# Kernel optimization log

Measured on AMD Instinct MI355X. Metric: run time of the kernel, lower is better.

The kernel has to match this reference:

```python
import math
import jax, jax.numpy as jnp
import numpy as np

N_TOKENS = 2048
HIDDEN = 2880
HEAD_DIM = 64
N_HEADS = 64          # total attention heads
N_KV = 8              # key/value heads
Q_MULT = N_HEADS // N_KV
SLIDING_WINDOW = 128  # layer_idx=0 (even) -> window active
ROPE_BASE = 150000.0
INIT_CTX = 4096.0
ROPE_SCALE = 32.0
NTK_ALPHA = 1.0
NTK_BETA = 32.0
QKV_DIM = HEAD_DIM * (N_HEADS + 2 * N_KV)  # 5120
EPS = 1e-5
NEG = -1e30


def _cos_sin(n_tokens):
    # YaRN-scaled rotary tables (scaling_factor > 1 branch)
    freq = ROPE_BASE ** (jnp.arange(0, HEAD_DIM, 2, dtype=jnp.float32) / HEAD_DIM)
    concentration = 0.1 * jnp.log(jnp.float32(ROPE_SCALE)) + 1.0
    d_half = HEAD_DIM / 2
    log_base = jnp.log(jnp.float32(ROPE_BASE))
    low = d_half * jnp.log(jnp.float32(INIT_CTX / (NTK_BETA * 2 * np.pi))) / log_base
    high = d_half * jnp.log(jnp.float32(INIT_CTX / (NTK_ALPHA * 2 * np.pi))) / log_base
    interpolation = 1.0 / (ROPE_SCALE * freq)
    extrapolation = 1.0 / freq
    ramp = (jnp.arange(d_half, dtype=jnp.float32) - low) / (high - low)
    mask = 1.0 - jnp.clip(ramp, 0.0, 1.0)
    inv_freq = interpolation * (1.0 - mask) + extrapolation * mask
    t = jnp.arange(n_tokens, dtype=jnp.float32)
    freqs = t[:, None] * inv_freq[None, :]          # [n, head_dim//2]
    return jnp.cos(freqs) * concentration, jnp.sin(freqs) * concentration


def _apply_rotary(x, cos, sin):
    # x: [n, heads, head_dim]; cos/sin: [n, head_dim//2]
    cos = cos[:, None, :].astype(x.dtype)
    sin = sin[:, None, :].astype(x.dtype)
    x1, x2 = jnp.split(x, 2, axis=-1)
    return jnp.concatenate((x1 * cos - x2 * sin, x2 * cos + x1 * sin), axis=-1)


def _rmsnorm(x, scale):
    t = x.astype(jnp.float32)
    rms = jnp.sqrt(jnp.mean(t * t, axis=-1, keepdims=True) + EPS)
    return (t / rms * scale).astype(x.dtype)


def _sdpa(q, k, v, sinks):
    # q: [n, h_kv, q_mult, d]; k, v: [n, h_kv, d]; sinks: [n_heads]
    n = q.shape[0]
    sm_scale = 1.0 / math.sqrt(HEAD_DIM)
    q32, k32, v32 = q.astype(jnp.float32), k.astype(jnp.float32), v.astype(jnp.float32)
    qk = jnp.einsum('qhmd,khd->hmqk', q32, k32) * jnp.float32(sm_scale)
    i = jnp.arange(n)
    # causal AND within sliding window: q - window < k <= q
    allowed = (i[None, :] <= i[:, None]) & (i[None, :] > i[:, None] - SLIDING_WINDOW)
    qk = qk + jnp.where(allowed, jnp.float32(0.0), jnp.float32(NEG))[None, None, :, :]
    s = sinks.astype(jnp.float32).reshape(N_KV, Q_MULT, 1, 1)
    s = jnp.broadcast_to(s, (N_KV, Q_MULT, n, 1))
    w = jax.nn.softmax(jnp.concatenate([qk, s], axis=-1), axis=-1)[..., :-1]
    attn = jnp.einsum('hmqk,khd->qhmd', w, v32)
    return attn.astype(q.dtype).reshape(n, -1)  # [n, n_heads*head_dim]


def setup_inputs() -> dict:
    key = jax.random.key(0)
    ks = jax.random.split(key, 5)
    s = 0.02
    return {
        'x': jax.random.normal(ks[0], (N_TOKENS, HIDDEN), jnp.float32),
        'norm_scale': jnp.ones((HIDDEN,), jnp.float32),
        'w_qkv': jax.random.normal(ks[1], (HIDDEN, QKV_DIM), jnp.float32) * s,
        'b_qkv': jnp.zeros((QKV_DIM,), jnp.float32),
        'sinks': jax.random.normal(ks[2], (N_HEADS,), jnp.float32),
        'w_out': jax.random.normal(ks[3], (N_HEADS * HEAD_DIM, HIDDEN), jnp.float32) * s,
        'b_out': jnp.zeros((HIDDEN,), jnp.float32),
    }


def reference(x, norm_scale, w_qkv, b_qkv, sinks, w_out, b_out):
    n = x.shape[0]
    t = _rmsnorm(x, norm_scale)
    qkv = t @ w_qkv + b_qkv                                   # [n, qkv_dim]
    q_end = N_HEADS * HEAD_DIM
    k_end = q_end + N_KV * HEAD_DIM
    q = qkv[:, :q_end].reshape(n, N_KV, Q_MULT, HEAD_DIM)
    k = qkv[:, q_end:k_end].reshape(n, N_KV, HEAD_DIM)
    v = qkv[:, k_end:].reshape(n, N_KV, HEAD_DIM)
    cos, sin = _cos_sin(n)
    q = _apply_rotary(q.reshape(n, -1, HEAD_DIM), cos, sin).reshape(n, N_KV, Q_MULT, HEAD_DIM)
    k = _apply_rotary(k, cos, sin)
    attn = _sdpa(q, k, v, sinks)                              # [n, n_heads*head_dim]
    return x + (attn @ w_out + b_out)
```

## Files before the change

kernel.cpp:

```cpp
#include <hip/hip_runtime.h>
#include <hip/hip_bf16.h>
#include <math.h>

#define N_TOK 2048
#define HIDDEN 2880
#define QKV_DIM 5120
#define LOG2E 1.44269504088896340736f

typedef __attribute__((ext_vector_type(8))) short short8;
typedef __attribute__((ext_vector_type(4))) float f32x4;
typedef __attribute__((ext_vector_type(16))) float f32x16;

__device__ __forceinline__ float bf2f(unsigned short u) {
  union { unsigned int i; float f; } c; c.i = ((unsigned int)u) << 16; return c.f;
}
__device__ __forceinline__ unsigned short f2bf(float f) {
  union { float f; unsigned int i; } c; c.f = f;
  unsigned int i = c.i;
  return (unsigned short)((i + 0x7FFFu + ((i >> 16) & 1u)) >> 16);
}
__device__ __forceinline__ void gload16(const void* g, void* l) {
  __builtin_amdgcn_global_load_lds((const __attribute__((address_space(1))) void*)g,
                                   (__attribute__((address_space(3))) void*)l, 16, 0, 0);
}

__global__ __launch_bounds__(256) void rmsnorm_kernel(
    const float* __restrict__ x, const float* __restrict__ scale,
    unsigned short* __restrict__ t)
{
  int row = blockIdx.x;
  const float* xr = x + (size_t)row * HIDDEN;
  float ss = 0.f;
  for (int i = threadIdx.x; i < HIDDEN / 4; i += 256) {
    float4 v = ((const float4*)xr)[i];
    ss += v.x * v.x + v.y * v.y + v.z * v.z + v.w * v.w;
  }
#pragma unroll
  for (int off = 32; off; off >>= 1) ss += __shfl_down(ss, off, 64);
  __shared__ float red[4];
  if ((threadIdx.x & 63) == 0) red[threadIdx.x >> 6] = ss;
  __syncthreads();
  float total = red[0] + red[1] + red[2] + red[3];
  float rinv = rsqrtf(total / (float)HIDDEN + 1e-5f);
  for (int i = threadIdx.x; i < HIDDEN / 4; i += 256) {
    float4 v = ((const float4*)xr)[i];
    float4 s4 = ((const float4*)scale)[i];
    union { unsigned short u[4]; uint2 p; } pk;
    pk.u[0] = f2bf(v.x * rinv * s4.x);
    pk.u[1] = f2bf(v.y * rinv * s4.y);
    pk.u[2] = f2bf(v.z * rinv * s4.z);
    pk.u[3] = f2bf(v.w * rinv * s4.w);
    *(uint2*)&t[(size_t)row * HIDDEN + i * 4] = pk.p;
  }
}

__global__ __launch_bounds__(256) void transpose_cast2(
    const float* __restrict__ inA, unsigned short* __restrict__ outA,
    const float* __restrict__ inB, unsigned short* __restrict__ outB)
{
  __shared__ float tile[64][65];
  int b = blockIdx.x;
  const float* in; unsigned short* out; int R, C, bx, by;
  if (b < 3600) { in = inA; out = outA; R = 2880; C = 5120; bx = b % 80; by = b / 80; }
  else { b -= 3600; in = inB; out = outB; R = 4096; C = 2880; bx = b % 45; by = b / 45; }
  const int r0 = by * 64, c0 = bx * 64;
  const int t = threadIdx.x;
  const int c4 = t & 15, rr = t >> 4;
#pragma unroll
  for (int p = 0; p < 4; ++p) {
    int row = rr + p * 16;
    float4 v = *(const float4*)&in[(size_t)(r0 + row) * C + c0 + c4 * 4];
    tile[row][c4 * 4 + 0] = v.x; tile[row][c4 * 4 + 1] = v.y;
    tile[row][c4 * 4 + 2] = v.z; tile[row][c4 * 4 + 3] = v.w;
  }
  __syncthreads();
  const int rc = t & 7;
#pragma unroll
  for (int it = 0; it < 2; ++it) {
    int cc = (t >> 3) + it * 32;
    unsigned short tmp[8];
#pragma unroll
    for (int i = 0; i < 8; ++i) tmp[i] = f2bf(tile[rc * 8 + i][cc]);
    *(uint4*)&out[(size_t)(c0 + cc) * R + r0 + rc * 8] = *(uint4*)tmp;
  }
}

template <int NF, int EPI>
__global__ __launch_bounds__(512, 2) void gemm8(
    const unsigned short* __restrict__ A,
    const unsigned short* __restrict__ Bt,
    const float* __restrict__ bias,
    const float* __restrict__ resid,
    void* __restrict__ Cout,
    int K, int Ncols)
{
  constexpr int BUFSZ = 16384 + NF * 8192;
  constexpr int NCH = 2 + NF;
  constexpr int HALF = NCH / 2;
  __shared__ char smem_[2 * BUFSZ];
  const int tid = threadIdx.x;
  const int lane = tid & 63;
  const int w = tid >> 6;
  const int fr = lane & 15, fq = lane >> 4;
  const int wr = w >> 2, wc = w & 3;

  const int nwg = gridDim.x;
  const int cpx = nwg >> 3;
  const int wg = (blockIdx.x & 7) * cpx + (blockIdx.x >> 3);
  const int by = wg & 15, bx = wg >> 4;
  const int row0 = by * 128, col0 = bx * (NF * 64);

  const unsigned short* gsrc[NCH];
  int ldsoff[NCH];
#pragma unroll
  for (int c = 0; c < NCH; ++c) {
    int g = tid + 512 * c;
    if (g < 1024) {
      int kk = g >> 9, rr = (g >> 2) & 127, u = g & 3;
      gsrc[c] = A + (size_t)(row0 + rr) * K + kk * 32 + ((u ^ ((rr >> 1) & 3)) * 8);
      ldsoff[c] = kk * 8192 + rr * 64 + u * 16;
    } else {
      int g2 = g - 1024;
      int kk = g2 / (NF * 256);
      int rm = g2 - kk * (NF * 256);
      int rr = rm >> 2, u = rm & 3;
      gsrc[c] = Bt + (size_t)(col0 + rr) * K + kk * 32 + ((u ^ ((rr >> 1) & 3)) * 8);
      ldsoff[c] = 16384 + kk * (NF * 4096) + rr * 64 + u * 16;
    }
  }
  const int urd = (fq ^ ((fr >> 1) & 3)) * 16;
  const int aoffb = (wr * 64 + fr) * 64 + urd;
  const int boffb = 16384 + (wc * NF * 16 + fr) * 64 + urd;

  f32x4 acc[4][NF];
#pragma unroll
  for (int mf = 0; mf < 4; ++mf)
#pragma unroll
    for (int nf = 0; nf < NF; ++nf) acc[mf][nf] = (f32x4)0.f;

  const int NT = K >> 6;

#define ISSUE(c) gload16(gsrc[c] + ktn, smem_ + nbufo + ldsoff[c])
#define RD_A(mf, kk) (*(const short8*)(smem_ + bufo + (kk)*8192 + (mf)*1024 + aoffb))
#define RD_B(nf, kk) (*(const short8*)(smem_ + bufo + (kk)*(NF*4096) + (nf)*1024 + boffb))

  {
    const int ktn = 0, nbufo = 0;
#pragma unroll
    for (int c = 0; c < NCH; ++c) gload16(gsrc[c] + ktn, smem_ + nbufo + ldsoff[c]);
  }

  for (int t = 0; t < NT; ++t) {
    const int bufo = (t & 1) * BUFSZ;
    const int nbufo = bufo ^ BUFSZ;
    const int ktn = (t + 1) * 64;
    const bool pref = (t + 1) < NT;

    asm volatile("s_waitcnt vmcnt(0)" ::: "memory");
    __builtin_amdgcn_s_barrier();

    if (pref) {
#pragma unroll
      for (int c = 0; c < HALF; ++c) ISSUE(c);
    }

    short8 afr[4], bfr[NF];
#pragma unroll
    for (int nf = 0; nf < NF; ++nf) bfr[nf] = RD_B(nf, 0);
#pragma unroll
    for (int mf = 0; mf < 4; ++mf) afr[mf] = RD_A(mf, 0);
    __builtin_amdgcn_s_setprio(1);
#pragma unroll
    for (int mf = 0; mf < 4; ++mf)
#pragma unroll
      for (int nf = 0; nf < NF; ++nf)
        acc[mf][nf] = __builtin_amdgcn_mfma_f32_16x16x32_bf16(afr[mf], bfr[nf], acc[mf][nf], 0, 0, 0);
    __builtin_amdgcn_s_setprio(0);

    if (pref) {
#pragma unroll
      for (int c = HALF; c < NCH; ++c) ISSUE(c);
    }

#pragma unroll
    for (int nf = 0; nf < NF; ++nf) bfr[nf] = RD_B(nf, 1);
#pragma unroll
    for (int mf = 0; mf < 4; ++mf) afr[mf] = RD_A(mf, 1);
    __builtin_amdgcn_s_setprio(1);
#pragma unroll
    for (int mf = 0; mf < 4; ++mf)
#pragma unroll
      for (int nf = 0; nf < NF; ++nf)
        acc[mf][nf] = __builtin_amdgcn_mfma_f32_16x16x32_bf16(afr[mf], bfr[nf], acc[mf][nf], 0, 0, 0);
    __builtin_amdgcn_s_setprio(0);
  }
#undef ISSUE
#undef RD_A
#undef RD_B

#pragma unroll
  for (int mf = 0; mf < 4; ++mf) {
#pragma unroll
    for (int nf = 0; nf < NF; ++nf) {
      const int colb = col0 + wc * NF * 16 + nf * 16 + fr;
      const int rowb = row0 + wr * 64 + mf * 16 + fq * 4;
      const float bs = bias[colb];
      if (EPI == 1) {
#pragma unroll
        for (int j = 0; j < 4; ++j)
          ((unsigned short*)Cout)[(size_t)(rowb + j) * Ncols + colb] =
              f2bf(acc[mf][nf][j] + bs);
      } else {
#pragma unroll
        for (int j = 0; j < 4; ++j) {
          const size_t idx = (size_t)(rowb + j) * Ncols + colb;
          ((float*)Cout)[idx] = acc[mf][nf][j] + bs + resid[idx];
        }
      }
    }
  }
}

__global__ __launch_bounds__(256) void rope_kernel(unsigned short* __restrict__ qkv)
{
  __shared__ float cs[32], sn[32];
  const int token = blockIdx.x;
  const int t = threadIdx.x;
  if (t < 32) {
    const float log_base = 11.9183905731f;
    float fj = (float)t;
    float extrap = expf(-log_base * fj * 0.03125f);
    float interp = extrap * 0.03125f;
    const float low  = 32.f * logf(4096.f / (32.f * 6.283185307179586f)) / log_base;
    const float high = 32.f * logf(4096.f / 6.283185307179586f) / log_base;
    float ramp = (fj - low) / (high - low);
    float maskv = 1.f - fminf(fmaxf(ramp, 0.f), 1.f);
    float inv_freq = interp * (1.f - maskv) + extrap * maskv;
    float ang = (float)token * inv_freq;
    const float conc = 1.3465735903f;
    float s, c;
    sincosf(ang, &s, &c);
    cs[t] = c * conc; sn[t] = s * conc;
  }
  __syncthreads();
  for (int p = t; p < 72 * 32; p += 256) {
    int h = p >> 5, j = p & 31;
    size_t base = (size_t)token * QKV_DIM + h * 64 + j;
    float c = cs[j], s = sn[j];
    float x1 = bf2f(qkv[base]), x2 = bf2f(qkv[base + 32]);
    qkv[base]      = f2bf(x1 * c - x2 * s);
    qkv[base + 32] = f2bf(x2 * c + x1 * s);
  }
}

__global__ __launch_bounds__(512) void attn_kernel(
    const unsigned short* __restrict__ qkv, const float* __restrict__ sinks,
    unsigned short* __restrict__ attn)
{
  __shared__ unsigned short Ks[160 * 64];
  __shared__ unsigned short Vt[64 * 192];
  const int tid  = threadIdx.x;
  const int lane = tid & 63;
  const int w    = tid >> 6;
  const int qb = blockIdx.x, kvh = blockIdx.y;
  const int q0 = qb * 32;
  const int kb = q0 - 128;
  const int h  = lane >> 5;
  const int ql = lane & 31;

  for (int it = w; it < 20; it += 8) {
    int r = it * 8 + (lane >> 3);
    int s = lane & 7;
    int j = kb + r; if (j < 0) j = 0;
    const unsigned short* src =
        qkv + (size_t)j * QKV_DIM + 4096 + kvh * 64 + ((s ^ (r & 7)) * 8);
    gload16(src, &Ks[r * 64 + s * 8]);
  }
  for (int c = tid; c < 2560; c += 512) {
    int jl = c >> 4;
    int d4 = (c & 15) * 4;
    int j = kb + jl; if (j < 0) j = 0;
    ushort4 v4 = *(const ushort4*)&qkv[(size_t)j * QKV_DIM + 4608 + kvh * 64 + d4];
    const unsigned short* pv = (const unsigned short*)&v4;
#pragma unroll
    for (int t = 0; t < 4; ++t) {
      int d = d4 + t;
      int slot = (jl >> 3) ^ (d & 7);
      Vt[d * 192 + slot * 8 + (jl & 7)] = pv[t];
    }
  }
  const int head = kvh * 8 + w;
  const int i_q = q0 + ql;
  short8 qf[4];
  {
    const unsigned short* qp = qkv + (size_t)i_q * QKV_DIM + head * 64 + h * 8;
#pragma unroll
    for (int ks = 0; ks < 4; ++ks) qf[ks] = *(const short8*)(qp + ks * 16);
  }
  __syncthreads();

  const float SC = 0.125f * LOG2E;
  f32x16 oacc0 = (f32x16)(0.f), oacc1 = (f32x16)(0.f);
  float m = -1e30f, l = 0.f;

  const int tstart = qb < 4 ? 4 - qb : 0;
  for (int tt = tstart; tt < 5; ++tt) {
    const int j0 = kb + tt * 32;
    f32x16 sacc = (f32x16)(0.f);
    const int kr = tt * 32 + ql;
#pragma unroll
    for (int ks = 0; ks < 4; ++ks) {
      short8 kf = *(const short8*)&Ks[kr * 64 + (((ks * 2 + h) ^ (kr & 7)) * 8)];
      sacc = __builtin_amdgcn_mfma_f32_32x32x16_bf16(kf, qf[ks], sacc, 0, 0, 0);
    }
    float sc16[16];
    float mt = -INFINITY;
#pragma unroll
    for (int e = 0; e < 16; ++e) {
      int kk = (e & 3) + 8 * (e >> 2) + 4 * h;
      int j = j0 + kk;
      float s2 = sacc[e] * SC;
      bool valid = (j <= i_q) && (j > i_q - 128);
      s2 = valid ? s2 : -INFINITY;
      sc16[e] = s2;
      mt = fmaxf(mt, s2);
    }
    mt = fmaxf(mt, __shfl_xor(mt, 32));
    float mnew = fmaxf(m, mt);
    float r = exp2f(m - mnew);
    l *= r;
    oacc0 *= r;
    oacc1 *= r;
    m = mnew;
    unsigned int wpk[8];
    float ls = 0.f;
#pragma unroll
    for (int e2 = 0; e2 < 8; ++e2) {
      float plo = exp2f(sc16[2 * e2]     - m);
      float phi = exp2f(sc16[2 * e2 + 1] - m);
      ls += plo + phi;
      asm("v_cvt_pk_bf16_f32 %0, %1, %2" : "=v"(wpk[e2]) : "v"(plo), "v"(phi));
    }
    l += ls;
#pragma unroll
    for (int m16 = 0; m16 < 2; ++m16) {
      int go = 2 * m16 + h;
      int gs = 2 * m16 + 1 - h;
      unsigned int x0 = (unsigned int)__shfl_xor((int)wpk[2 * gs],     32);
      unsigned int x1 = (unsigned int)__shfl_xor((int)wpk[2 * gs + 1], 32);
      union { unsigned int u[4]; short8 s; } bu;
      bu.u[0] = h ? x0 : wpk[2 * go];
      bu.u[1] = h ? x1 : wpk[2 * go + 1];
      bu.u[2] = h ? wpk[2 * go]     : x0;
      bu.u[3] = h ? wpk[2 * go + 1] : x1;
      short8 bfrag = bu.s;
#pragma unroll
      for (int dt = 0; dt < 2; ++dt) {
        int d = dt * 32 + ql;
        int slot = (tt * 4 + m16 * 2 + h) ^ (d & 7);
        short8 vf = *(const short8*)&Vt[d * 192 + slot * 8];
        if (dt == 0)
          oacc0 = __builtin_amdgcn_mfma_f32_32x32x16_bf16(vf, bfrag, oacc0, 0, 0, 0);
        else
          oacc1 = __builtin_amdgcn_mfma_f32_32x32x16_bf16(vf, bfrag, oacc1, 0, 0, 0);
      }
    }
  }
  float lt = l + __shfl_xor(l, 32);
  lt += exp2f(sinks[head] * LOG2E - m);
  float inv = 1.f / lt;
  unsigned short* op = attn + (size_t)i_q * 4096 + head * 64;
#pragma unroll
  for (int dt = 0; dt < 2; ++dt) {
#pragma unroll
    for (int g = 0; g < 4; ++g) {
      float f0, f1, f2, f3;
      if (dt == 0) {
        f0 = oacc0[4 * g]; f1 = oacc0[4 * g + 1]; f2 = oacc0[4 * g + 2]; f3 = oacc0[4 * g + 3];
      } else {
        f0 = oacc1[4 * g]; f1 = oacc1[4 * g + 1]; f2 = oacc1[4 * g + 2]; f3 = oacc1[4 * g + 3];
      }
      unsigned int u0, u1;
      asm("v_cvt_pk_bf16_f32 %0, %1, %2" : "=v"(u0) : "v"(f0 * inv), "v"(f1 * inv));
      asm("v_cvt_pk_bf16_f32 %0, %1, %2" : "=v"(u1) : "v"(f2 * inv), "v"(f3 * inv));
      int d = dt * 32 + 8 * g + 4 * h;
      uint2 pr; pr.x = u0; pr.y = u1;
      *(uint2*)(op + d) = pr;
    }
  }
}

extern "C" void kernel_launch(void* const* d_in, const int* in_sizes, int n_in,
                              void* d_out, int out_size, void* d_ws, size_t ws_size,
                              hipStream_t stream)
{
  const float* x      = (const float*)d_in[0];
  const float* nscale = (const float*)d_in[1];
  const float* w_qkv  = (const float*)d_in[2];
  const float* b_qkv  = (const float*)d_in[3];
  const float* sinks  = (const float*)d_in[4];
  const float* w_out  = (const float*)d_in[5];
  const float* b_out  = (const float*)d_in[6];

  char* ws = (char*)d_ws;
  unsigned short* t_bf  = (unsigned short*)(ws);
  unsigned short* wqkvT = (unsigned short*)(ws + 11796480);
  unsigned short* qkv   = (unsigned short*)(ws + 41287680);
  unsigned short* attn  = (unsigned short*)(ws + 62259200);
  unsigned short* woutT = (unsigned short*)(ws + 79036416);

  rmsnorm_kernel<<<N_TOK, 256, 0, stream>>>(x, nscale, t_bf);
  transpose_cast2<<<6480, 256, 0, stream>>>(w_qkv, wqkvT, w_out, woutT);
  gemm8<5, 1><<<256, 512, 0, stream>>>(t_bf, wqkvT, b_qkv, nullptr, (void*)qkv, 2880, 5120);
  rope_kernel<<<N_TOK, 256, 0, stream>>>(qkv);
  attn_kernel<<<dim3(64, 8), 512, 0, stream>>>(qkv, sinks, attn);
  gemm8<3, 2><<<240, 512, 0, stream>>>(attn, woutT, b_out, x, d_out, 4096, 2880);
}
```

Measured before the change: 187.0 us.

## Load GEMM B operand directly from global into registers, bypassing LDS

The GEMM no longer stages the weight (B) tile through shared memory. Each wave loads its B fragments straight from global memory into registers, double-buffered across iterations through a manually unrolled lambda body, and only A still goes through LDS. This cuts the shared-memory footprint and LDS read traffic for B. The cost is that each wave fetches B with uncoalesced-ish per-lane 16-byte loads, and B rows shared by waves in the same column are re-read from global/L2 instead of being reused from LDS.

Measured after the change: 326.1 us. 1.74x slower.

```diff
diff --git a/kernel.cpp b/kernel.cpp
--- a/kernel.cpp
+++ b/kernel.cpp
@@ -86,7 +86,7 @@
 }
 
 template <int NF, int EPI>
-__global__ __launch_bounds__(512, 2) void gemm8(
+__global__ __launch_bounds__(512, 2) void gemm9(
     const unsigned short* __restrict__ A,
     const unsigned short* __restrict__ Bt,
     const float* __restrict__ bias,
@@ -94,10 +94,7 @@
     void* __restrict__ Cout,
     int K, int Ncols)
 {
-  constexpr int BUFSZ = 16384 + NF * 8192;
-  constexpr int NCH = 2 + NF;
-  constexpr int HALF = NCH / 2;
-  __shared__ char smem_[2 * BUFSZ];
+  __shared__ char smem_[32768];
   const int tid = threadIdx.x;
   const int lane = tid & 63;
   const int w = tid >> 6;
@@ -110,27 +107,22 @@
   const int by = wg & 15, bx = wg >> 4;
   const int row0 = by * 128, col0 = bx * (NF * 64);
 
-  const unsigned short* gsrc[NCH];
-  int ldsoff[NCH];
-#pragma unroll
-  for (int c = 0; c < NCH; ++c) {
+  const unsigned short* gsrcA[2];
+  int ldsoffA[2];
+#pragma unroll
+  for (int c = 0; c < 2; ++c) {
     int g = tid + 512 * c;
-    if (g < 1024) {
-      int kk = g >> 9, rr = (g >> 2) & 127, u = g & 3;
-      gsrc[c] = A + (size_t)(row0 + rr) * K + kk * 32 + ((u ^ ((rr >> 1) & 3)) * 8);
-      ldsoff[c] = kk * 8192 + rr * 64 + u * 16;
-    } else {
-      int g2 = g - 1024;
-      int kk = g2 / (NF * 256);
-      int rm = g2 - kk * (NF * 256);
-      int rr = rm >> 2, u = rm & 3;
-      gsrc[c] = Bt + (size_t)(col0 + rr) * K + kk * 32 + ((u ^ ((rr >> 1) & 3)) * 8);
-      ldsoff[c] = 16384 + kk * (NF * 4096) + rr * 64 + u * 16;
-    }
+    int kk = g >> 9, rr = (g >> 2) & 127, u = g & 3;
+    gsrcA[c] = A + (size_t)(row0 + rr) * K + kk * 32 + ((u ^ ((rr >> 1) & 3)) * 8);
+    ldsoffA[c] = kk * 8192 + rr * 64 + u * 16;
   }
   const int urd = (fq ^ ((fr >> 1) & 3)) * 16;
   const int aoffb = (wr * 64 + fr) * 64 + urd;
-  const int boffb = 16384 + (wc * NF * 16 + fr) * 64 + urd;
+
+  const unsigned short* Brow[NF];
+#pragma unroll
+  for (int nf = 0; nf < NF; ++nf)
+    Brow[nf] = Bt + (size_t)(col0 + wc * NF * 16 + nf * 16 + fr) * K + fq * 8;
 
   f32x4 acc[4][NF];
 #pragma unroll
@@ -140,63 +132,57 @@
 
   const int NT = K >> 6;
 
-#define ISSUE(c) gload16(gsrc[c] + ktn, smem_ + nbufo + ldsoff[c])
-#define RD_A(mf, kk) (*(const short8*)(smem_ + bufo + (kk)*8192 + (mf)*1024 + aoffb))
-#define RD_B(nf, kk) (*(const short8*)(smem_ + bufo + (kk)*(NF*4096) + (nf)*1024 + boffb))
-
-  {
-    const int ktn = 0, nbufo = 0;
-#pragma unroll
-    for (int c = 0; c < NCH; ++c) gload16(gsrc[c] + ktn, smem_ + nbufo + ldsoff[c]);
-  }
-
-  for (int t = 0; t < NT; ++t) {
-    const int bufo = (t & 1) * BUFSZ;
-    const int nbufo = bufo ^ BUFSZ;
-    const int ktn = (t + 1) * 64;
-    const bool pref = (t + 1) < NT;
-
+  short8 bA[NF * 2], bB[NF * 2];
+
+#pragma unroll
+  for (int c = 0; c < 2; ++c) gload16(gsrcA[c], smem_ + ldsoffA[c]);
+#pragma unroll
+  for (int nf = 0; nf < NF; ++nf) {
+    bA[nf * 2 + 0] = *(const short8*)(Brow[nf] + 0);
+    bA[nf * 2 + 1] = *(const short8*)(Brow[nf] + 32);
+  }
+
+  auto body = [&](int T, short8 (&BC)[NF * 2], short8 (&BN)[NF * 2]) {
+    const int bufo = (T & 1) * 16384;
+    const int nbufo = bufo ^ 16384;
+    const int ktn = (T + 1) * 64;
     asm volatile("s_waitcnt vmcnt(0)" ::: "memory");
     __builtin_amdgcn_s_barrier();
-
-    if (pref) {
-#pragma unroll
-      for (int c = 0; c < HALF; ++c) ISSUE(c);
-    }
-
-    short8 afr[4], bfr[NF];
-#pragma unroll
-    for (int nf = 0; nf < NF; ++nf) bfr[nf] = RD_B(nf, 0);
-#pragma unroll
-    for (int mf = 0; mf < 4; ++mf) afr[mf] = RD_A(mf, 0);
+    if (T + 1 < NT) {
+#pragma unroll
+      for (int c = 0; c < 2; ++c) gload16(gsrcA[c] + ktn, smem_ + nbufo + ldsoffA[c]);
+#pragma unroll
+      for (int nf = 0; nf < NF; ++nf) {
+        BN[nf * 2 + 0] = *(const short8*)(Brow[nf] + ktn);
+        BN[nf * 2 + 1] = *(const short8*)(Brow[nf] + ktn + 32);
+      }
+    }
+    short8 afr[4];
+#pragma unroll
+    for (int mf = 0; mf < 4; ++mf)
+      afr[mf] = *(const short8*)(smem_ + bufo + mf * 1024 + aoffb);
     __builtin_amdgcn_s_setprio(1);
 #pragma unroll
     for (int mf = 0; mf < 4; ++mf)
 #pragma unroll
       for (int nf = 0; nf < NF; ++nf)
-        acc[mf][nf] = __builtin_amdgcn_mfma_f32_16x16x32_bf16(afr[mf], bfr[nf], acc[mf][nf], 0, 0, 0);
+        acc[mf][nf] = __builtin_amdgcn_mfma_f32_16x16x32_bf16(afr[mf], BC[nf * 2 + 0], acc[mf][nf], 0, 0, 0);
     __builtin_amdgcn_s_setprio(0);
-
-    if (pref) {
-#pragma unroll
-      for (int c = HALF; c < NCH; ++c) ISSUE(c);
-    }
-
-#pragma unroll
-    for (int nf = 0; nf < NF; ++nf) bfr[nf] = RD_B(nf, 1);
-#pragma unroll
-    for (int mf = 0; mf < 4; ++mf) afr[mf] = RD_A(mf, 1);
+#pragma unroll
+    for (int mf = 0; mf < 4; ++mf)
+      afr[mf] = *(const short8*)(smem_ + bufo + 8192 + mf * 1024 + aoffb);
     __builtin_amdgcn_s_setprio(1);
 #pragma unroll
     for (int mf = 0; mf < 4; ++mf)
 #pragma unroll
       for (int nf = 0; nf < NF; ++nf)
-        acc[mf][nf] = __builtin_amdgcn_mfma_f32_16x16x32_bf16(afr[mf], bfr[nf], acc[mf][nf], 0, 0, 0);
+        acc[mf][nf] = __builtin_amdgcn_mfma_f32_16x16x32_bf16(afr[mf], BC[nf * 2 + 1], acc[mf][nf], 0, 0, 0);
     __builtin_amdgcn_s_setprio(0);
-  }
-#undef ISSUE
-#undef RD_A
-#undef RD_B
+  };
+
+  int t = 0;
+  for (; t + 2 <= NT; t += 2) { body(t, bA, bB); body(t + 1, bB, bA); }
+  if (t < NT) body(t, bA, bB);
 
 #pragma unroll
   for (int mf = 0; mf < 4; ++mf) {
@@ -411,8 +397,8 @@
 
   rmsnorm_kernel<<<N_TOK, 256, 0, stream>>>(x, nscale, t_bf);
   transpose_cast2<<<6480, 256, 0, stream>>>(w_qkv, wqkvT, w_out, woutT);
-  gemm8<5, 1><<<256, 512, 0, stream>>>(t_bf, wqkvT, b_qkv, nullptr, (void*)qkv, 2880, 5120);
+  gemm9<5, 1><<<256, 512, 0, stream>>>(t_bf, wqkvT, b_qkv, nullptr, (void*)qkv, 2880, 5120);
   rope_kernel<<<N_TOK, 256, 0, stream>>>(qkv);
   attn_kernel<<<dim3(64, 8), 512, 0, stream>>>(qkv, sinks, attn);
-  gemm8<3, 2><<<240, 512, 0, stream>>>(attn, woutT, b_out, x, d_out, 4096, 2880);
-}
+  gemm9<3, 2><<<240, 512, 0, stream>>>(attn, woutT, b_out, x, d_out, 4096, 2880);
+}
```
